# Optimization experiments

Measured on AMD Instinct MI355X. Metric: run time of the kernel, lower is better.

Reference implementation:

```python
import jax, jax.numpy as jnp
import numpy as np

B, T, IN, H, L = 64, 50, 256, 2000, 11  # L layers: 1 stem + 5 residual blocks of 2
EPS = 1e-4  # BatchNorm eps from module


def setup_inputs() -> dict:
    key = jax.random.key(0)
    ks = jax.random.split(key, 6)
    x = jax.random.normal(ks[0], (B, T, IN), jnp.float32)
    # InputMapping Linear weights, init uniform(-0.001, 0.001) per init_ih default
    W0 = jax.random.uniform(ks[1], (H, IN), jnp.float32, -0.001, 0.001)
    b0 = jnp.zeros((H,), jnp.float32)
    # recurrent diagonal weights, clipped to |u| <= hidden_max_abs=2
    u0 = jax.random.uniform(ks[2], (H,), jnp.float32, -1.0, 1.0)
    g0 = jnp.ones((H,), jnp.float32)   # BN gamma (shared across timesteps)
    be0 = jnp.zeros((H,), jnp.float32)  # BN beta
    Ws = jax.random.uniform(ks[3], (L - 1, H, H), jnp.float32, -0.001, 0.001)
    bs = jnp.zeros((L - 1, H), jnp.float32)
    us = jax.random.uniform(ks[4], (L - 1, H), jnp.float32, -1.0, 1.0)
    gs = jnp.ones((L - 1, H), jnp.float32)
    bes = jnp.zeros((L - 1, H), jnp.float32)
    return dict(x=x, W0=W0, b0=b0, u0=u0, g0=g0, be0=be0,
                Ws=Ws, bs=bs, us=us, gs=gs, bes=bes)


def _indrnn_layer(x, W, b, u, g, be):
    """InputMapping Linear -> per-timestep BatchNorm -> IndRNN scan (relu).
    x: (B,T,D) -> (B,T,H)"""
    m = jnp.einsum('btd,hd->bth', x, W) + b           # Linear per timestep
    mu = m.mean(axis=0, keepdims=True)                 # BN stats over batch, per (t, c)
    var = m.var(axis=0, keepdims=True)
    m = (m - mu) * jax.lax.rsqrt(var + EPS) * g + be

    def step(h, xt):
        h = jax.nn.relu(xt + u * h)                    # diagonal recurrence
        return h, h

    h0 = jnp.zeros((x.shape[0], u.shape[0]), x.dtype)
    _, hs = jax.lax.scan(step, h0, jnp.swapaxes(m, 0, 1))  # scan over time
    return jnp.swapaxes(hs, 0, 1)


def reference(x, W0, b0, u0, g0, be0, Ws, bs, us, gs, bes):
    # stem layer (input_size -> hidden)
    out = _indrnn_layer(x, W0, b0, u0, g0, be0)
    # residual blocks of residual_layers=2 with identity skip
    n = Ws.shape[0]  # 10
    i = 0
    while i < n:
        res = out
        out = _indrnn_layer(out, Ws[i], bs[i], us[i], gs[i], bes[i])
        if i + 1 < n:
            out = _indrnn_layer(out, Ws[i + 1], bs[i + 1], us[i + 1], gs[i + 1], bes[i + 1])
        out = out + res
        i += 2
    return out
```

## Files before the change

### kernel.cpp

```cpp
#include <hip/hip_runtime.h>

typedef unsigned short u16;
typedef __attribute__((ext_vector_type(8))) short bf16x8;
typedef __attribute__((ext_vector_type(4))) float f32x4;

#define NB 64
#define NT 50
#define NIN 256
#define NH 2000
#define HP 2048
#define EPS 1e-4f

__device__ __forceinline__ u16 f2bf(float f) {
  unsigned x = __float_as_uint(f);
  x += 0x7fffu + ((x >> 16) & 1u);
  return (u16)(x >> 16);
}
__device__ __forceinline__ float bf2f(u16 u) {
  return __uint_as_float(((unsigned)u) << 16);
}

#define GLDS16(g, l) __builtin_amdgcn_global_load_lds( \
  (const __attribute__((address_space(1))) unsigned int*)(g), \
  (__attribute__((address_space(3))) unsigned int*)(l), 16, 0, 0)

__global__ __launch_bounds__(256)
void cvt_all_kernel(const float* __restrict__ x, const float* __restrict__ W0,
                    const float* __restrict__ Ws, u16* __restrict__ x16,
                    u16* __restrict__ W016, u16* __restrict__ Ws16) {
  int bid = blockIdx.x;
  union { u16 u[8]; uint4 v; } o;
  if (bid < 400) {
    int tid = bid * 256 + threadIdx.x;
    int row = tid >> 5;
    int c8  = (tid & 31) << 3;
    int t = row >> 6, b = row & 63;
    const float* src = x + (size_t)(b * NT + t) * NIN + c8;
    float4 a = *(const float4*)src;
    float4 c = *(const float4*)(src + 4);
    o.u[0]=f2bf(a.x); o.u[1]=f2bf(a.y); o.u[2]=f2bf(a.z); o.u[3]=f2bf(a.w);
    o.u[4]=f2bf(c.x); o.u[5]=f2bf(c.y); o.u[6]=f2bf(c.z); o.u[7]=f2bf(c.w);
    *(uint4*)(x16 + (size_t)row * NIN + c8) = o.v;
  } else if (bid < 656) {
    int tid = (bid - 400) * 256 + threadIdx.x;
    int r = tid >> 5;
    int c8 = (tid & 31) << 3;
    if (r < NH) {
      const float* src = W0 + (size_t)r * NIN + c8;
      float4 a = *(const float4*)src;
      float4 b = *(const float4*)(src + 4);
      o.u[0]=f2bf(a.x); o.u[1]=f2bf(a.y); o.u[2]=f2bf(a.z); o.u[3]=f2bf(a.w);
      o.u[4]=f2bf(b.x); o.u[5]=f2bf(b.y); o.u[6]=f2bf(b.z); o.u[7]=f2bf(b.w);
    } else {
      o.v = make_uint4(0,0,0,0);
    }
    *(uint4*)(W016 + (size_t)tid * 8) = o.v;
  } else {
    int tid = (bid - 656) * 256 + threadIdx.x;
    int l  = tid >> 19;
    int r  = (tid >> 8) & 2047;
    int c8 = (tid & 255) << 3;
    if (r < NH && c8 < NH) {
      const float* src = Ws + (size_t)l * (NH * NH) + (size_t)r * NH + c8;
      float4 a = *(const float4*)src;
      float4 b = *(const float4*)(src + 4);
      o.u[0]=f2bf(a.x); o.u[1]=f2bf(a.y); o.u[2]=f2bf(a.z); o.u[3]=f2bf(a.w);
      o.u[4]=f2bf(b.x); o.u[5]=f2bf(b.y); o.u[6]=f2bf(b.z); o.u[7]=f2bf(b.w);
    } else {
      o.v = make_uint4(0,0,0,0);
    }
    *(uint4*)(Ws16 + (size_t)tid * 8) = o.v;
  }
}

__global__ __launch_bounds__(512, 4)
void gemm_bn_kernel(const u16* __restrict__ A, const u16* __restrict__ W,
                    u16* __restrict__ Mn, const float* __restrict__ g,
                    const float* __restrict__ be, int K) {
  __shared__ u16 As[2 * 128 * 64];
  __shared__ u16 Bs[2 * 128 * 64];
  const int tid = threadIdx.x;
  const int w = tid >> 6, l = tid & 63;
  const int wm = w >> 2, wn = w & 3;
  const int bid = blockIdx.x;
  const int xcd = bid & 7;
  const int r0  = bid >> 3;
  const int hi  = r0 >= 25;
  const int bn  = xcd + (hi << 3);
  const int bm  = r0 - 25 * hi;
  f32x4 acc[4][2] = {};
  const u16* Ab = A + (size_t)bm * 128 * K;
  const u16* Wb = W + (size_t)bn * 128 * K;

  const int rib  = l >> 3;
  const int scbs = (l & 7) ^ rib;
  const size_t goff1 = (size_t)((2 * w    ) * 8 + rib) * K + scbs * 8;
  const size_t goff2 = (size_t)((2 * w + 1) * 8 + rib) * K + scbs * 8;
  const int lr  = l & 15;
  const int lkb = l >> 4;
  const int nk  = K >> 6;

#define STAGE(tt, bi) do {                                              \
    GLDS16(Ab + goff1 + (tt) * 64, As + (bi) * 8192 + (2*w    ) * 512); \
    GLDS16(Ab + goff2 + (tt) * 64, As + (bi) * 8192 + (2*w + 1) * 512); \
    GLDS16(Wb + goff1 + (tt) * 64, Bs + (bi) * 8192 + (2*w    ) * 512); \
    GLDS16(Wb + goff2 + (tt) * 64, Bs + (bi) * 8192 + (2*w + 1) * 512); \
  } while (0)

  STAGE(0, 0);
  asm volatile("s_waitcnt vmcnt(0)" ::: "memory");
  __builtin_amdgcn_s_barrier();

  int p = 0;
  for (int t = 0; t < nk; ++t) {
    if (t + 1 < nk) STAGE(t + 1, p ^ 1);
    const u16* Ac = As + p * 8192;
    const u16* Bc = Bs + p * 8192;
#pragma unroll
    for (int kk = 0; kk < 2; ++kk) {
      bf16x8 af[4], bfr[2];
      const int cb = ((kk * 4 + lkb) ^ (lr & 7)) * 8;
#pragma unroll
      for (int i = 0; i < 4; ++i)
        af[i] = *(const bf16x8*)(Ac + (wm * 64 + i * 16 + lr) * 64 + cb);
#pragma unroll
      for (int j = 0; j < 2; ++j)
        bfr[j] = *(const bf16x8*)(Bc + (wn * 32 + j * 16 + lr) * 64 + cb);
      __builtin_amdgcn_s_setprio(1);
#pragma unroll
      for (int i = 0; i < 4; ++i)
#pragma unroll
        for (int j = 0; j < 2; ++j)
          acc[i][j] = __builtin_amdgcn_mfma_f32_16x16x32_bf16(af[i], bfr[j], acc[i][j], 0, 0, 0);
      __builtin_amdgcn_s_setprio(0);
    }
    asm volatile("s_waitcnt vmcnt(0)" ::: "memory");
    __builtin_amdgcn_s_barrier();
    p ^= 1;
  }
#undef STAGE

  const int lg = l >> 4;
  const int rbase = bm * 128 + wm * 64;
  const int cbase = bn * 128 + wn * 32;
#pragma unroll
  for (int j = 0; j < 2; ++j) {
    float s = 0.f, s2 = 0.f;
#pragma unroll
    for (int i = 0; i < 4; ++i)
#pragma unroll
      for (int r = 0; r < 4; ++r) { float v = acc[i][j][r]; s += v; s2 += v * v; }
    s  += __shfl_xor(s, 16);  s2 += __shfl_xor(s2, 16);
    s  += __shfl_xor(s, 32);  s2 += __shfl_xor(s2, 32);
    float mu  = s * (1.f / 64.f);
    float var = fmaxf(s2 * (1.f / 64.f) - mu * mu, 0.f);
    int col = cbase + j * 16 + lr;
    bool ok = col < NH;
    float gg = ok ? g[col]  : 0.f;
    float bb = ok ? be[col] : 0.f;
    float sc = rsqrtf(var + EPS) * gg;
#pragma unroll
    for (int i = 0; i < 4; ++i) {
      int row0 = rbase + i * 16 + lg * 4;
#pragma unroll
      for (int r = 0; r < 4; ++r)
        Mn[(size_t)(row0 + r) * HP + col] = f2bf((acc[i][j][r] - mu) * sc + bb);
    }
  }
}

__device__ __forceinline__ void pad16(u16* out16, int b, int h) {
#pragma unroll
  for (int t = 0; t < NT; ++t)
    *(unsigned*)(out16 + (size_t)(t * NB + b) * HP + h) = 0u;
}

__global__ void scan_a_kernel(const u16* __restrict__ Mn, const float* __restrict__ u,
                              u16* __restrict__ out16) {
  int tid = blockIdx.x * 256 + threadIdx.x;
  int h2 = tid & 1023, b = tid >> 10;
  int h = h2 << 1;
  if (h >= NH) { pad16(out16, b, h); return; }
  unsigned mv[NT];
#pragma unroll
  for (int t = 0; t < NT; ++t)
    mv[t] = *(const unsigned*)(Mn + (size_t)(t * NB + b) * HP + h);
  float2 uu = *(const float2*)(u + h);
  float h0 = 0.f, h1 = 0.f;
#pragma unroll
  for (int t = 0; t < NT; ++t) {
    h0 = fmaxf(fmaf(uu.x, h0, bf2f((u16)(mv[t] & 0xffffu))), 0.f);
    h1 = fmaxf(fmaf(uu.y, h1, bf2f((u16)(mv[t] >> 16))), 0.f);
    *(unsigned*)(out16 + (size_t)(t * NB + b) * HP + h) =
        (unsigned)f2bf(h0) | ((unsigned)f2bf(h1) << 16);
  }
}

template<bool HASRES>
__global__ void scan_b_kernel(const u16* __restrict__ Mn, const float* __restrict__ u,
                              const u16* __restrict__ res16, u16* __restrict__ out16) {
  int tid = blockIdx.x * 256 + threadIdx.x;
  int h2 = tid & 1023, b = tid >> 10;
  int h = h2 << 1;
  if (h >= NH) { pad16(out16, b, h); return; }
  unsigned mv[NT];
#pragma unroll
  for (int t = 0; t < NT; ++t)
    mv[t] = *(const unsigned*)(Mn + (size_t)(t * NB + b) * HP + h);
  unsigned rv[NT];
  if (HASRES) {
#pragma unroll
    for (int t = 0; t < NT; ++t)
      rv[t] = *(const unsigned*)(res16 + (size_t)(t * NB + b) * HP + h);
  }
  float2 uu = *(const float2*)(u + h);
  float h0 = 0.f, h1 = 0.f;
#pragma unroll
  for (int t = 0; t < NT; ++t) {
    h0 = fmaxf(fmaf(uu.x, h0, bf2f((u16)(mv[t] & 0xffffu))), 0.f);
    h1 = fmaxf(fmaf(uu.y, h1, bf2f((u16)(mv[t] >> 16))), 0.f);
    float o0 = h0, o1 = h1;
    if (HASRES) {
      o0 += bf2f((u16)(rv[t] & 0xffffu));
      o1 += bf2f((u16)(rv[t] >> 16));
    }
    *(unsigned*)(out16 + (size_t)(t * NB + b) * HP + h) =
        (unsigned)f2bf(o0) | ((unsigned)f2bf(o1) << 16);
  }
}

__global__ void scan_c_kernel(const u16* __restrict__ Mn, const float* __restrict__ u,
                              const u16* __restrict__ res16, float* __restrict__ out) {
  int tid = blockIdx.x * 256 + threadIdx.x;
  int h2 = tid & 1023, b = tid >> 10;
  int h = h2 << 1;
  if (h >= NH) return;
  unsigned mv[NT];
#pragma unroll
  for (int t = 0; t < NT; ++t)
    mv[t] = *(const unsigned*)(Mn + (size_t)(t * NB + b) * HP + h);
  unsigned rv[NT];
#pragma unroll
  for (int t = 0; t < NT; ++t)
    rv[t] = *(const unsigned*)(res16 + (size_t)(t * NB + b) * HP + h);
  float2 uu = *(const float2*)(u + h);
  float h0 = 0.f, h1 = 0.f;
#pragma unroll
  for (int t = 0; t < NT; ++t) {
    h0 = fmaxf(fmaf(uu.x, h0, bf2f((u16)(mv[t] & 0xffffu))), 0.f);
    h1 = fmaxf(fmaf(uu.y, h1, bf2f((u16)(mv[t] >> 16))), 0.f);
    *(float2*)(out + (size_t)(b * NT + t) * NH + h) =
        make_float2(h0 + bf2f((u16)(rv[t] & 0xffffu)),
                    h1 + bf2f((u16)(rv[t] >> 16)));
  }
}

extern "C" void kernel_launch(void* const* d_in, const int* in_sizes, int n_in,
                              void* d_out, int out_size, void* d_ws, size_t ws_size,
                              hipStream_t stream) {
  const float* x   = (const float*)d_in[0];
  const float* W0  = (const float*)d_in[1];
  const float* u0  = (const float*)d_in[3];
  const float* g0  = (const float*)d_in[4];
  const float* be0 = (const float*)d_in[5];
  const float* Ws  = (const float*)d_in[6];
  const float* us  = (const float*)d_in[8];
  const float* gs  = (const float*)d_in[9];
  const float* bes = (const float*)d_in[10];
  float* out = (float*)d_out;

  char* ws = (char*)d_ws;
  u16*   x16  = (u16*)  (ws + 0);
  u16*   W016 = (u16*)  (ws + 1638400);
  u16*   Ws16 = (u16*)  (ws + 2686976);
  u16*   Mbuf = (u16*)  (ws + 86573056);
  u16*   A16  = (u16*)  (ws + 99680256);
  u16*   B16  = (u16*)  (ws + 112787456);

  cvt_all_kernel<<<21136, 256, 0, stream>>>(x, W0, Ws, x16, W016, Ws16);

  gemm_bn_kernel<<<400, 512, 0, stream>>>(x16, W016, Mbuf, g0, be0, NIN);
  scan_b_kernel<false><<<256, 256, 0, stream>>>(Mbuf, u0, nullptr, A16);

  for (int l = 0; l < 10; ++l) {
    const u16* Ain = (l & 1) ? B16 : A16;
    gemm_bn_kernel<<<400, 512, 0, stream>>>(Ain, Ws16 + (size_t)l * HP * HP, Mbuf,
                                            gs + (size_t)l * NH, bes + (size_t)l * NH, HP);
    const float* ul = us + (size_t)l * NH;
    if ((l & 1) == 0) {
      scan_a_kernel<<<256, 256, 0, stream>>>(Mbuf, ul, B16);
    } else if (l < 9) {
      scan_b_kernel<true><<<256, 256, 0, stream>>>(Mbuf, ul, A16, A16);
    } else {
      scan_c_kernel<<<256, 256, 0, stream>>>(Mbuf, ul, A16, out);
    }
  }
}
```

Measured before the change: 504.3 us.

## Load GEMM B operand directly into registers, bypassing LDS staging

```diff
diff --git a/kernel.cpp b/kernel.cpp
--- a/kernel.cpp
+++ b/kernel.cpp
@@ -78,7 +78,6 @@
                     u16* __restrict__ Mn, const float* __restrict__ g,
                     const float* __restrict__ be, int K) {
   __shared__ u16 As[2 * 128 * 64];
-  __shared__ u16 Bs[2 * 128 * 64];
   const int tid = threadIdx.x;
   const int w = tid >> 6, l = tid & 63;
   const int wm = w >> 2, wn = w & 3;
@@ -100,45 +99,60 @@
   const int lkb = l >> 4;
   const int nk  = K >> 6;
 
-#define STAGE(tt, bi) do {                                              \
+  const u16* Bf = Wb + (size_t)(wn * 32 + lr) * K + lkb * 8;
+
+#define STAGEA(tt, bi) do {                                             \
     GLDS16(Ab + goff1 + (tt) * 64, As + (bi) * 8192 + (2*w    ) * 512); \
     GLDS16(Ab + goff2 + (tt) * 64, As + (bi) * 8192 + (2*w + 1) * 512); \
-    GLDS16(Wb + goff1 + (tt) * 64, Bs + (bi) * 8192 + (2*w    ) * 512); \
-    GLDS16(Wb + goff2 + (tt) * 64, Bs + (bi) * 8192 + (2*w + 1) * 512); \
   } while (0)
 
-  STAGE(0, 0);
+#define LOADB(bset, tt) do {                                            \
+    bset[0][0] = *(const bf16x8*)(Bf           + (tt) * 64);            \
+    bset[0][1] = *(const bf16x8*)(Bf           + (tt) * 64 + 32);       \
+    bset[1][0] = *(const bf16x8*)(Bf + 16 * K  + (tt) * 64);            \
+    bset[1][1] = *(const bf16x8*)(Bf + 16 * K  + (tt) * 64 + 32);       \
+  } while (0)
+
+#define COMPUTE(bi, bset) do {                                          \
+    const u16* Ac = As + (bi) * 8192;                                   \
+    _Pragma("unroll")                                                   \
+    for (int kk = 0; kk < 2; ++kk) {                                    \
+      bf16x8 af[4];                                                     \
+      const int cb = ((kk * 4 + lkb) ^ (lr & 7)) * 8;                   \
+      _Pragma("unroll")                                                 \
+      for (int i = 0; i < 4; ++i)                                       \
+        af[i] = *(const bf16x8*)(Ac + (wm * 64 + i * 16 + lr) * 64 + cb); \
+      __builtin_amdgcn_s_setprio(1);                                    \
+      _Pragma("unroll")                                                 \
+      for (int i = 0; i < 4; ++i)                                       \
+        _Pragma("unroll")                                               \
+        for (int j = 0; j < 2; ++j)                                     \
+          acc[i][j] = __builtin_amdgcn_mfma_f32_16x16x32_bf16(          \
+              af[i], bset[j][kk], acc[i][j], 0, 0, 0);                  \
+      __builtin_amdgcn_s_setprio(0);                                    \
+    }                                                                   \
+  } while (0)
+
+  bf16x8 b0[2][2], b1[2][2];
+
+  LOADB(b0, 0);
+  STAGEA(0, 0);
   asm volatile("s_waitcnt vmcnt(0)" ::: "memory");
   __builtin_amdgcn_s_barrier();
 
-  int p = 0;
-  for (int t = 0; t < nk; ++t) {
-    if (t + 1 < nk) STAGE(t + 1, p ^ 1);
-    const u16* Ac = As + p * 8192;
-    const u16* Bc = Bs + p * 8192;
-#pragma unroll
-    for (int kk = 0; kk < 2; ++kk) {
-      bf16x8 af[4], bfr[2];
-      const int cb = ((kk * 4 + lkb) ^ (lr & 7)) * 8;
-#pragma unroll
-      for (int i = 0; i < 4; ++i)
-        af[i] = *(const bf16x8*)(Ac + (wm * 64 + i * 16 + lr) * 64 + cb);
-#pragma unroll
-      for (int j = 0; j < 2; ++j)
-        bfr[j] = *(const bf16x8*)(Bc + (wn * 32 + j * 16 + lr) * 64 + cb);
-      __builtin_amdgcn_s_setprio(1);
-#pragma unroll
-      for (int i = 0; i < 4; ++i)
-#pragma unroll
-        for (int j = 0; j < 2; ++j)
-          acc[i][j] = __builtin_amdgcn_mfma_f32_16x16x32_bf16(af[i], bfr[j], acc[i][j], 0, 0, 0);
-      __builtin_amdgcn_s_setprio(0);
-    }
+  for (int t = 0; t < nk; t += 2) {
+    if (t + 1 < nk) { LOADB(b1, t + 1); STAGEA(t + 1, 1); }
+    COMPUTE(0, b0);
     asm volatile("s_waitcnt vmcnt(0)" ::: "memory");
     __builtin_amdgcn_s_barrier();
-    p ^= 1;
-  }
-#undef STAGE
+    if (t + 2 < nk) { LOADB(b0, t + 2); STAGEA(t + 2, 0); }
+    COMPUTE(1, b1);
+    asm volatile("s_waitcnt vmcnt(0)" ::: "memory");
+    __builtin_amdgcn_s_barrier();
+  }
+#undef STAGEA
+#undef LOADB
+#undef COMPUTE
 
   const int lg = l >> 4;
   const int rbase = bm * 128 + wm * 64;
```

After: 861.7 us. 70.9% more time.
